# Performance work log

Measured on AMD Instinct MI355X. Metric: run time of the kernel, lower is better.

## Reference

```python
import jax, jax.numpy as jnp
import numpy as np

H = 2048      # hidden_size
I = 768       # moe_intermediate_size
E = 32        # num_experts
K = 8         # num_experts_per_tok (top_k)
T = 1024      # tokens (batch * seq)


def setup_inputs() -> dict:
    key = jax.random.key(0)
    k1, k2, k3, k4 = jax.random.split(key, 4)
    return {
        "hidden_states": jax.random.normal(k1, (T, H), jnp.float32),
        "gate_weight": jax.random.normal(k2, (E, H), jnp.float32) * 0.02,
        "w13_weight": jax.random.normal(k3, (E, 2 * I, H), jnp.float32) * 0.02,
        "w2_weight": jax.random.normal(k4, (E, H, I), jnp.float32) * 0.02,
    }


def reference(hidden_states, gate_weight, w13_weight, w2_weight):
    x = hidden_states  # [T, H]
    # --- router (Qwen3MoeSparseMoeBlock gating) ---
    logits = x @ gate_weight.T                      # [T, E]
    probs = jax.nn.softmax(logits, axis=-1)
    topk_w, topk_idx = jax.lax.top_k(probs, K)      # [T, K]
    topk_w = topk_w / jnp.sum(topk_w, axis=-1, keepdims=True)  # norm_topk_prob
    # dense combine matrix [T, E]: routing weight per (token, expert), 0 if not selected
    combine = jnp.zeros((x.shape[0], E), x.dtype).at[
        jnp.arange(x.shape[0])[:, None], topk_idx
    ].add(topk_w)
    # --- expert FFNs (fused gate+up = w13, SiLU-gated, then w2 down-proj) ---
    h = jnp.einsum('th,eoh->eto', x, w13_weight)    # [E, T, 2I]
    gate, up = h[:, :, :I], h[:, :, I:]
    act = jax.nn.silu(gate) * up                    # [E, T, I]
    y = jnp.einsum('eti,ehi->eth', act, w2_weight)  # [E, T, H]
    # --- weighted combine ---
    return jnp.einsum('eth,te->th', y, combine)     # [T, H]
```

## Files before the change

### kernel.cpp

```cpp
#include <hip/hip_runtime.h>
#include <hip/hip_bf16.h>
#include <math.h>

#define T_TOK 1024
#define H_DIM 2048
#define I_DIM 768
#define E_NUM 32
#define K_TOP 8
#define BK 32
#define GRID_P 1024

typedef __bf16 bf16x8 __attribute__((ext_vector_type(8)));
typedef float  f32x4  __attribute__((ext_vector_type(4)));

__device__ __forceinline__ bf16x8 cvt2_bf16(const f32x4 a, const f32x4 b) {
    bf16x8 r;
    r[0] = (__bf16)a[0]; r[1] = (__bf16)a[1]; r[2] = (__bf16)a[2]; r[3] = (__bf16)a[3];
    r[4] = (__bf16)b[0]; r[5] = (__bf16)b[1]; r[6] = (__bf16)b[2]; r[7] = (__bf16)b[3];
    return r;
}

__device__ __forceinline__ int frag_off(int r, int kgrp8) {
    return (r >> 4) * 512 + kgrp8 * 128 + (r & 15) * 8;
}

__global__ __launch_bounds__(256) void router_kernel(
    const float* __restrict__ x, const float* __restrict__ gw,
    float* __restrict__ wdense, unsigned int* __restrict__ masks,
    __bf16* __restrict__ xb)
{
    const int t = blockIdx.x;
    const int tid = threadIdx.x;
    __shared__ float part[256];
    __shared__ float logits[E_NUM];

    {
        const float* xr2 = x + (size_t)t * H_DIM + tid * 8;
        const f32x4 a = *(const f32x4*)(xr2);
        const f32x4 b = *(const f32x4*)(xr2 + 4);
        *(bf16x8*)(xb + (size_t)t * H_DIM + tid * 8) = cvt2_bf16(a, b);
    }

    const int e = tid & 31;
    const int chunk = tid >> 5;
    const float* xr = x + (size_t)t * H_DIM;
    const float* gr = gw + (size_t)e * H_DIM;
    const int base = chunk * (H_DIM / 8);
    float s = 0.f;
    for (int h = 0; h < H_DIM / 8; h += 4) {
        const f32x4 xv = *reinterpret_cast<const f32x4*>(xr + base + h);
        const f32x4 gv = *reinterpret_cast<const f32x4*>(gr + base + h);
        s += xv[0]*gv[0] + xv[1]*gv[1] + xv[2]*gv[2] + xv[3]*gv[3];
    }
    part[tid] = s;
    __syncthreads();
    if (tid < E_NUM) {
        float tot = 0.f;
        for (int c = 0; c < 8; ++c) tot += part[c * 32 + tid];
        logits[tid] = tot;
    }
    __syncthreads();
    if (tid == 0) {
        float l[E_NUM];
        for (int i = 0; i < E_NUM; ++i) {
            l[i] = logits[i];
            wdense[(size_t)t * E_NUM + i] = 0.f;
        }
        unsigned mask = 0;
        int   idx[K_TOP];
        float lv[K_TOP];
        for (int k = 0; k < K_TOP; ++k) {
            float best = -1e30f; int bi = 0;
            for (int i = 0; i < E_NUM; ++i)
                if (!((mask >> i) & 1u) && l[i] > best) { best = l[i]; bi = i; }
            mask |= (1u << bi); idx[k] = bi; lv[k] = best;
        }
        const float m = lv[0];
        float den = 0.f;
        for (int k = 0; k < K_TOP; ++k) den += expf(lv[k] - m);
        for (int k = 0; k < K_TOP; ++k)
            wdense[(size_t)t * E_NUM + idx[k]] = expf(lv[k] - m) / den;
        masks[t] = mask;
    }
}

__global__ __launch_bounds__(256) void count_kernel(
    const unsigned int* __restrict__ masks, int* __restrict__ cnt)
{
    const int e = blockIdx.x;
    const int tid = threadIdx.x;
    int c = 0;
    for (int t = tid; t < T_TOK; t += 256) c += (masks[t] >> e) & 1u;
    __shared__ int red[256];
    red[tid] = c; __syncthreads();
    for (int s = 128; s > 0; s >>= 1) {
        if (tid < s) red[tid] += red[tid + s];
        __syncthreads();
    }
    if (tid == 0) cnt[e] = red[0];
}

__global__ void scan_kernel(const int* __restrict__ cnt, int* __restrict__ off,
                            int* __restrict__ tbl)
{
    if (threadIdx.x == 0 && blockIdx.x == 0) {
        int r = 0, nt = 0;
        for (int e = 0; e < E_NUM; ++e) {
            off[e] = r;
            const int c = cnt[e];
            r += c;
            const int t = (c + 127) >> 7;
            for (int z = 0; z < t; ++z) tbl[1 + nt++] = (e << 8) | z;
        }
        tbl[0] = nt;
    }
}

__global__ __launch_bounds__(256) void fill_kernel(
    const unsigned int* __restrict__ masks, const float* __restrict__ wdense,
    const int* __restrict__ off, int* __restrict__ tok, float* __restrict__ wgt,
    int* __restrict__ posl)
{
    const int e = blockIdx.x;
    const int tid = threadIdx.x;
    const int PER = T_TOK / 256;
    int sel[PER]; int c = 0;
    for (int i = 0; i < PER; ++i) {
        const int t = tid * PER + i;
        sel[i] = (masks[t] >> e) & 1u;
        c += sel[i];
    }
    __shared__ int s[256];
    s[tid] = c; __syncthreads();
    if (tid == 0) {
        int r = 0;
        for (int j = 0; j < 256; ++j) { int v = s[j]; s[j] = r; r += v; }
    }
    __syncthreads();
    int pos = off[e] + s[tid];
    for (int i = 0; i < PER; ++i) {
        if (sel[i]) {
            const int t = tid * PER + i;
            tok[pos] = t;
            wgt[pos] = wdense[(size_t)t * E_NUM + e];
            const int slot = __popc(masks[t] & ((1u << e) - 1u));
            posl[t * K_TOP + slot] = pos;
            pos++;
        }
    }
}

#define GEMM_PHASE(P, Q)                                                       \
  {                                                                            \
    if (scur + 2 < NS) {                                                       \
      const int kk = (scur + 2) * BK;                                          \
      pa##P##_0 = *(const bf16x8*)(ap + kk);                                   \
      pa##P##_1 = *(const bf16x8*)(ap + kk + 8);                               \
      pb##P##_0 = *(const f32x4*)(wp + kk);                                    \
      pb##P##_1 = *(const f32x4*)(wp + kk + 4);                                \
      pb##P##_2 = *(const f32x4*)(wp + kk + 8);                                \
      pb##P##_3 = *(const f32x4*)(wp + kk + 12);                               \
    }                                                                          \
    bf16x8 af[4], bfr[4];                                                      \
    _Pragma("unroll")                                                          \
    for (int m = 0; m < 4; ++m)                                                \
      af[m] = *(const bf16x8*)&As[P][((wm >> 4) + m) * 512 + lane * 8];        \
    _Pragma("unroll")                                                          \
    for (int n = 0; n < 4; ++n)                                                \
      bfr[n] = *(const bf16x8*)&Bs[P][(wn * 4 + n) * 512 + lane * 8];          \
    _Pragma("unroll")                                                          \
    for (int m = 0; m < 4; ++m)                                                \
      _Pragma("unroll")                                                        \
      for (int n = 0; n < 4; ++n)                                              \
        acc[m][n] = __builtin_amdgcn_mfma_f32_16x16x32_bf16(af[m], bfr[n],     \
                                                            acc[m][n], 0,0,0); \
    if (scur + 1 < NS) {                                                       \
      *(bf16x8*)&As[Q][wo]       = pa##Q##_0;                                  \
      *(bf16x8*)&As[Q][wo + 128] = pa##Q##_1;                                  \
      *(bf16x8*)&Bs[Q][wo]       = cvt2_bf16(pb##Q##_0, pb##Q##_1);            \
      *(bf16x8*)&Bs[Q][wo + 128] = cvt2_bf16(pb##Q##_2, pb##Q##_3);            \
    }                                                                          \
    asm volatile("s_waitcnt lgkmcnt(0)" ::: "memory");                         \
    __builtin_amdgcn_s_barrier();                                              \
    ++scur;                                                                    \
  }

#define GEMM_PROLOGUE()                                                        \
    pa0_0 = *(const bf16x8*)(ap);                                              \
    pa0_1 = *(const bf16x8*)(ap + 8);                                          \
    pb0_0 = *(const f32x4*)(wp);                                               \
    pb0_1 = *(const f32x4*)(wp + 4);                                           \
    pb0_2 = *(const f32x4*)(wp + 8);                                           \
    pb0_3 = *(const f32x4*)(wp + 12);                                          \
    pa1_0 = *(const bf16x8*)(ap + BK);                                         \
    pa1_1 = *(const bf16x8*)(ap + BK + 8);                                     \
    pb1_0 = *(const f32x4*)(wp + BK);                                          \
    pb1_1 = *(const f32x4*)(wp + BK + 4);                                      \
    pb1_2 = *(const f32x4*)(wp + BK + 8);                                      \
    pb1_3 = *(const f32x4*)(wp + BK + 12);                                     \
    *(bf16x8*)&As[0][wo]       = pa0_0;                                        \
    *(bf16x8*)&As[0][wo + 128] = pa0_1;                                        \
    *(bf16x8*)&Bs[0][wo]       = cvt2_bf16(pb0_0, pb0_1);                      \
    *(bf16x8*)&Bs[0][wo + 128] = cvt2_bf16(pb0_2, pb0_3);                      \
    asm volatile("s_waitcnt lgkmcnt(0)" ::: "memory");                         \
    __builtin_amdgcn_s_barrier();

__global__ __launch_bounds__(256, 3) void gemm1_kernel(
    const __bf16* __restrict__ xb, const float* __restrict__ w13,
    const int* __restrict__ tok, const int* __restrict__ cnt,
    const int* __restrict__ off, const int* __restrict__ tbl,
    unsigned short* __restrict__ act)
{
    __shared__ __bf16 As[2][4096];
    __shared__ __bf16 Bs[2][4096];
    const int tid  = threadIdx.x;
    const int wid  = tid >> 6;
    const int lane = tid & 63;
    const int wm = (wid >> 1) * 64;
    const int wn = (wid & 1);
    const int lrow = lane & 15;
    const int sr = tid >> 1;
    const int kh = tid & 1;
    const int wo = frag_off(sr, kh * 2);
    const int NS = H_DIM / BK;

    const int W = tbl[0] * 12;
    for (int w = blockIdx.x; w < W; w += gridDim.x) {
        const int ti   = w / 12;
        const int nidx = w - ti * 12;
        const int ez = tbl[1 + ti];
        const int e  = ez >> 8;
        const int m0 = (ez & 255) * 128;
        const int c  = cnt[e];
        const int o  = off[e];
        const int n0 = nidx * 64;

        int rA = m0 + sr; rA = rA < c ? rA : c - 1;
        const __bf16* ap = xb + (size_t)tok[o + rA] * H_DIM + kh * 16;
        const int grp = sr >> 5;
        const int wrow = (grp & 1) * I_DIM + n0 + (grp >> 1) * 32 + (sr & 31);
        const float* wp = w13 + (size_t)e * (2 * I_DIM) * H_DIM
                              + (size_t)wrow * H_DIM + kh * 16;

        bf16x8 pa0_0, pa0_1, pa1_0, pa1_1;
        f32x4  pb0_0, pb0_1, pb0_2, pb0_3, pb1_0, pb1_1, pb1_2, pb1_3;
        f32x4  acc[4][4] = {};

        GEMM_PROLOGUE()

        int scur = 0;
        for (int it = 0; it < NS; it += 2) {
            GEMM_PHASE(0, 1)
            GEMM_PHASE(1, 0)
        }

#pragma unroll
        for (int m = 0; m < 4; ++m)
#pragma unroll
            for (int n = 0; n < 2; ++n)
#pragma unroll
                for (int i = 0; i < 4; ++i) {
                    const int row = m0 + wm + m * 16 + (lane >> 4) * 4 + i;
                    if (row < c) {
                        const int icol = n0 + wn * 32 + n * 16 + lrow;
                        const float g = acc[m][n][i];
                        const float u = acc[m][n + 2][i];
                        const float a = (g / (1.f + expf(-g))) * u;
                        act[(size_t)(o + row) * I_DIM + icol] =
                            __builtin_bit_cast(unsigned short, (__bf16)a);
                    }
                }
    }
}

__global__ __launch_bounds__(256, 3) void gemm2_kernel(
    const unsigned short* __restrict__ act, const float* __restrict__ w2,
    const int* __restrict__ tok, const float* __restrict__ wgt,
    const int* __restrict__ cnt, const int* __restrict__ off,
    const int* __restrict__ tbl, unsigned short* __restrict__ ybuf)
{
    __shared__ __bf16 As[2][4096];
    __shared__ __bf16 Bs[2][4096];
    const int tid  = threadIdx.x;
    const int wid  = tid >> 6;
    const int lane = tid & 63;
    const int wm = (wid >> 1) * 64;
    const int wn = (wid & 1);
    const int lrow = lane & 15;
    const int sr = tid >> 1;
    const int kh = tid & 1;
    const int wo = frag_off(sr, kh * 2);
    const int NS = I_DIM / BK;

    const int W = tbl[0] * 16;
    for (int w = blockIdx.x; w < W; w += gridDim.x) {
        const int ti   = w >> 4;
        const int nidx = w & 15;
        const int ez = tbl[1 + ti];
        const int e  = ez >> 8;
        const int m0 = (ez & 255) * 128;
        const int c  = cnt[e];
        const int o  = off[e];
        const int n0 = nidx * 128;

        int rA = m0 + sr; rA = rA < c ? rA : c - 1;
        const __bf16* ap = (const __bf16*)act + (size_t)(o + rA) * I_DIM + kh * 16;
        const float* wp = w2 + (size_t)e * H_DIM * I_DIM
                             + (size_t)(n0 + sr) * I_DIM + kh * 16;

        bf16x8 pa0_0, pa0_1, pa1_0, pa1_1;
        f32x4  pb0_0, pb0_1, pb0_2, pb0_3, pb1_0, pb1_1, pb1_2, pb1_3;
        f32x4  acc[4][4] = {};

        GEMM_PROLOGUE()

        int scur = 0;
        for (int it = 0; it < NS; it += 2) {
            GEMM_PHASE(0, 1)
            GEMM_PHASE(1, 0)
        }

#pragma unroll
        for (int m = 0; m < 4; ++m)
#pragma unroll
            for (int i = 0; i < 4; ++i) {
                const int row = m0 + wm + m * 16 + (lane >> 4) * 4 + i;
                if (row < c) {
                    const float wv = wgt[o + row];
                    unsigned short* yr = ybuf + (size_t)(o + row) * H_DIM
                                              + n0 + wn * 64 + lrow;
#pragma unroll
                    for (int n = 0; n < 4; ++n)
                        yr[n * 16] = __builtin_bit_cast(
                            unsigned short, (__bf16)(wv * acc[m][n][i]));
                }
            }
    }
}

__global__ __launch_bounds__(256) void combine_kernel(
    const unsigned short* __restrict__ ybuf, const int* __restrict__ posl,
    float* __restrict__ out)
{
    const int t = blockIdx.x;
    int p[K_TOP];
#pragma unroll
    for (int s = 0; s < K_TOP; ++s) p[s] = posl[t * K_TOP + s];
    const int h0 = threadIdx.x * 8;
    float a[8] = {};
#pragma unroll
    for (int s = 0; s < K_TOP; ++s) {
        const bf16x8 v = *(const bf16x8*)(ybuf + (size_t)p[s] * H_DIM + h0);
#pragma unroll
        for (int j = 0; j < 8; ++j) a[j] += (float)v[j];
    }
    f32x4 o0 = {a[0], a[1], a[2], a[3]};
    f32x4 o1 = {a[4], a[5], a[6], a[7]};
    *(f32x4*)(out + (size_t)t * H_DIM + h0)     = o0;
    *(f32x4*)(out + (size_t)t * H_DIM + h0 + 4) = o1;
}

extern "C" void kernel_launch(void* const* d_in, const int* in_sizes, int n_in,
                              void* d_out, int out_size, void* d_ws, size_t ws_size,
                              hipStream_t stream)
{
    const float* x   = (const float*)d_in[0];
    const float* gw  = (const float*)d_in[1];
    const float* w13 = (const float*)d_in[2];
    const float* w2  = (const float*)d_in[3];
    float* out = (float*)d_out;

    char* ws = (char*)d_ws;
    float*          wdense = (float*)(ws + 0x00000);
    unsigned int*   masks  = (unsigned int*)(ws + 0x20000);
    int*            cnt    = (int*)(ws + 0x21000);
    int*            off    = (int*)(ws + 0x21800);
    int*            tbl    = (int*)(ws + 0x22000);
    int*            tok    = (int*)(ws + 0x23000);
    float*          wgt    = (float*)(ws + 0x2B000);
    unsigned short* act    = (unsigned short*)(ws + 0x33000);
    __bf16*         xb     = (__bf16*)(ws + 0xC40000);
    int*            posl   = (int*)(ws + 0x1040000);
    unsigned short* ybuf   = (unsigned short*)(ws + 0x1100000);

    router_kernel<<<T_TOK, 256, 0, stream>>>(x, gw, wdense, masks, xb);
    count_kernel<<<E_NUM, 256, 0, stream>>>(masks, cnt);
    scan_kernel<<<1, 64, 0, stream>>>(cnt, off, tbl);
    fill_kernel<<<E_NUM, 256, 0, stream>>>(masks, wdense, off, tok, wgt, posl);
    gemm1_kernel<<<GRID_P, 256, 0, stream>>>(xb, w13, tok, cnt, off, tbl, act);
    gemm2_kernel<<<GRID_P, 256, 0, stream>>>(act, w2, tok, wgt, cnt, off, tbl, ybuf);
    combine_kernel<<<T_TOK, 256, 0, stream>>>(ybuf, posl, out);
}
```

Baseline: 336.8 us.

## Fuse count, scan and fill into one ballot-based route kernel; raise MFMA priority

Replaces three small routing kernels (count, serial scan, fill) with one 1024-thread block that uses wave ballots and popcounts to count tokens per expert, compute offsets and scatter token indices, weights and positions. This removes two kernel launches and the serial per-expert work of the old fill kernel. Separately, the GEMM inner loop wraps the MFMA block in s_setprio(1)/s_setprio(0) so the matrix-core issue gets scheduling priority over the other waves' memory work. The routing output ordering within an expert stays by token index, so downstream kernels are unchanged.

```diff
diff --git a/kernel.cpp b/kernel.cpp
--- a/kernel.cpp
+++ b/kernel.cpp
@@ -84,68 +84,56 @@
     }
 }
 
-__global__ __launch_bounds__(256) void count_kernel(
-    const unsigned int* __restrict__ masks, int* __restrict__ cnt)
-{
-    const int e = blockIdx.x;
-    const int tid = threadIdx.x;
-    int c = 0;
-    for (int t = tid; t < T_TOK; t += 256) c += (masks[t] >> e) & 1u;
-    __shared__ int red[256];
-    red[tid] = c; __syncthreads();
-    for (int s = 128; s > 0; s >>= 1) {
-        if (tid < s) red[tid] += red[tid + s];
-        __syncthreads();
-    }
-    if (tid == 0) cnt[e] = red[0];
-}
-
-__global__ void scan_kernel(const int* __restrict__ cnt, int* __restrict__ off,
-                            int* __restrict__ tbl)
-{
-    if (threadIdx.x == 0 && blockIdx.x == 0) {
+__global__ __launch_bounds__(1024) void route_kernel(
+    const unsigned int* __restrict__ masks, const float* __restrict__ wdense,
+    int* __restrict__ cnt, int* __restrict__ off, int* __restrict__ tbl,
+    int* __restrict__ tok, float* __restrict__ wgt, int* __restrict__ posl)
+{
+    const int tid  = threadIdx.x;
+    const int wv   = tid >> 6;
+    const int lane = tid & 63;
+    __shared__ int wcnt[E_NUM][16];
+    __shared__ int woff[E_NUM][16];
+    __shared__ int eoff[E_NUM];
+    __shared__ int ecnt[E_NUM];
+
+    const unsigned int m = masks[tid];
+#pragma unroll
+    for (int e = 0; e < E_NUM; ++e) {
+        const unsigned long long b = __ballot((m >> e) & 1u);
+        if (lane == 0) wcnt[e][wv] = __popcll(b);
+    }
+    __syncthreads();
+    if (tid < E_NUM) {
+        int r = 0;
+        for (int w = 0; w < 16; ++w) { woff[tid][w] = r; r += wcnt[tid][w]; }
+        ecnt[tid] = r;
+    }
+    __syncthreads();
+    if (tid == 0) {
         int r = 0, nt = 0;
         for (int e = 0; e < E_NUM; ++e) {
-            off[e] = r;
-            const int c = cnt[e];
+            eoff[e] = r; off[e] = r;
+            const int c = ecnt[e];
+            cnt[e] = c;
             r += c;
-            const int t = (c + 127) >> 7;
-            for (int z = 0; z < t; ++z) tbl[1 + nt++] = (e << 8) | z;
+            const int nz = (c + 127) >> 7;
+            for (int z = 0; z < nz; ++z) tbl[1 + nt++] = (e << 8) | z;
         }
         tbl[0] = nt;
     }
-}
-
-__global__ __launch_bounds__(256) void fill_kernel(
-    const unsigned int* __restrict__ masks, const float* __restrict__ wdense,
-    const int* __restrict__ off, int* __restrict__ tok, float* __restrict__ wgt,
-    int* __restrict__ posl)
-{
-    const int e = blockIdx.x;
-    const int tid = threadIdx.x;
-    const int PER = T_TOK / 256;
-    int sel[PER]; int c = 0;
-    for (int i = 0; i < PER; ++i) {
-        const int t = tid * PER + i;
-        sel[i] = (masks[t] >> e) & 1u;
-        c += sel[i];
-    }
-    __shared__ int s[256];
-    s[tid] = c; __syncthreads();
-    if (tid == 0) {
-        int r = 0;
-        for (int j = 0; j < 256; ++j) { int v = s[j]; s[j] = r; r += v; }
-    }
-    __syncthreads();
-    int pos = off[e] + s[tid];
-    for (int i = 0; i < PER; ++i) {
-        if (sel[i]) {
-            const int t = tid * PER + i;
-            tok[pos] = t;
-            wgt[pos] = wdense[(size_t)t * E_NUM + e];
-            const int slot = __popc(masks[t] & ((1u << e) - 1u));
-            posl[t * K_TOP + slot] = pos;
-            pos++;
+    __syncthreads();
+#pragma unroll
+    for (int e = 0; e < E_NUM; ++e) {
+        const int bit = (m >> e) & 1u;
+        const unsigned long long b = __ballot(bit);
+        if (bit) {
+            const int pos = eoff[e] + woff[e][wv]
+                          + (int)__popcll(b & ((1ULL << lane) - 1ULL));
+            tok[pos] = tid;
+            wgt[pos] = wdense[(size_t)tid * E_NUM + e];
+            const int slot = __popc(m & ((1u << e) - 1u));
+            posl[tid * K_TOP + slot] = pos;
         }
     }
 }
@@ -168,12 +156,14 @@
     _Pragma("unroll")                                                          \
     for (int n = 0; n < 4; ++n)                                                \
       bfr[n] = *(const bf16x8*)&Bs[P][(wn * 4 + n) * 512 + lane * 8];          \
+    __builtin_amdgcn_s_setprio(1);                                             \
     _Pragma("unroll")                                                          \
     for (int m = 0; m < 4; ++m)                                                \
       _Pragma("unroll")                                                        \
       for (int n = 0; n < 4; ++n)                                              \
         acc[m][n] = __builtin_amdgcn_mfma_f32_16x16x32_bf16(af[m], bfr[n],     \
                                                             acc[m][n], 0,0,0); \
+    __builtin_amdgcn_s_setprio(0);                                             \
     if (scur + 1 < NS) {                                                       \
       *(bf16x8*)&As[Q][wo]       = pa##Q##_0;                                  \
       *(bf16x8*)&As[Q][wo + 128] = pa##Q##_1;                                  \
@@ -384,9 +374,7 @@
     unsigned short* ybuf   = (unsigned short*)(ws + 0x1100000);
 
     router_kernel<<<T_TOK, 256, 0, stream>>>(x, gw, wdense, masks, xb);
-    count_kernel<<<E_NUM, 256, 0, stream>>>(masks, cnt);
-    scan_kernel<<<1, 64, 0, stream>>>(cnt, off, tbl);
-    fill_kernel<<<E_NUM, 256, 0, stream>>>(masks, wdense, off, tok, wgt, posl);
+    route_kernel<<<1, 1024, 0, stream>>>(masks, wdense, cnt, off, tbl, tok, wgt, posl);
     gemm1_kernel<<<GRID_P, 256, 0, stream>>>(xb, w13, tok, cnt, off, tbl, act);
     gemm2_kernel<<<GRID_P, 256, 0, stream>>>(act, w2, tok, wgt, cnt, off, tbl, ybuf);
     combine_kernel<<<T_TOK, 256, 0, stream>>>(ybuf, posl, out);
```

Result: no change. 337.7 us (+0.3%).
